# Optimization experiments

Measured on AMD Instinct MI355X. Metric: run time of the kernel, lower is better.

The kernel has to match this reference:

```python
import jax, jax.numpy as jnp
import numpy as np

N_QUBITS = 12
DEPTH = 4
OUT_DIM = 4096
BATCH = 2048
M_IN = 4096


def setup_inputs() -> dict:
    key = jax.random.key(0)
    k1, k2 = jax.random.split(key)
    x = jax.random.normal(k1, (BATCH, M_IN), dtype=jnp.float32)
    w = jax.random.uniform(k2, (DEPTH, N_QUBITS, 3), dtype=jnp.float32) * (2.0 * np.pi)
    return {"x": x, "w": w}


def _rot_matrix(phi, theta, omega):
    # PennyLane Rot(phi, theta, omega) = RZ(omega) @ RY(theta) @ RZ(phi)
    c = jnp.cos(theta / 2)
    s = jnp.sin(theta / 2)
    m = jnp.stack([
        jnp.stack([jnp.exp(-1j * (phi + omega) / 2) * c, -jnp.exp(1j * (phi - omega) / 2) * s]),
        jnp.stack([jnp.exp(-1j * (phi - omega) / 2) * s, jnp.exp(1j * (phi + omega) / 2) * c]),
    ])
    return m.astype(jnp.complex64)


def _apply_1q(s, U, q):
    # s: (B,) + (2,)*n ; wire q lives on axis q+1 (wire 0 = MSB, default.qubit order)
    s = jnp.moveaxis(s, q + 1, -1)
    s = jnp.einsum('...j,ij->...i', s, U)
    return jnp.moveaxis(s, -1, q + 1)


def _cnot(s, c, t):
    # control wire c < target wire t; flip target axis on the control=1 slice
    p0 = s[(slice(None),) * (c + 1) + (0,)]
    p1 = jnp.flip(s[(slice(None),) * (c + 1) + (1,)], axis=t)  # axis t after removing axis c+1
    return jnp.stack([p0, p1], axis=c + 1)


def _layer(s, wl):
    n = N_QUBITS
    for i in range(n):
        s = _apply_1q(s, _rot_matrix(wl[i, 0], wl[i, 1], wl[i, 2]), i)
    for i in range(n):
        for j in range(i + 1, n):
            s = _cnot(s, i, j)
    return s


def reference(x, w):
    B, m = x.shape
    n = N_QUBITS
    # amplitude embedding: per-sample L2 normalize with uniform fallback
    norm = jnp.linalg.norm(x, axis=1, keepdims=True)
    ok = norm > 1e-10
    amp = jnp.where(ok, x / jnp.where(ok, norm, 1.0), 1.0 / np.sqrt(m))
    s = amp.astype(jnp.complex64).reshape((B,) + (2,) * n)
    for layer in range(DEPTH):
        s = _layer(s, w[layer])
    sv = s.reshape(B, -1)
    probs = sv.real ** 2 + sv.imag ** 2
    pn = probs[:, :OUT_DIM]
    tot = jnp.sum(pn, axis=1, keepdims=True)
    okp = tot > 1e-10
    out = jnp.where(okp, pn / jnp.where(okp, tot, 1.0), 1.0 / OUT_DIM)
    return out.astype(x.dtype)
```

## Files before the change

### kernel.cpp

```cpp
#include <hip/hip_runtime.h>
#include <math.h>

#define NQ 12
#define DIM 4096
#define NLAYER 4
#define NT 256

typedef float v2 __attribute__((ext_vector_type(2)));

__device__ __forceinline__ v2 mkv2(float a, float b) { v2 r; r.x = a; r.y = b; return r; }
__device__ __forceinline__ v2 sp(float a) { v2 r; r.x = a; r.y = a; return r; }
__device__ __forceinline__ v2 pkfma(v2 a, float b, v2 c) {
  return __builtin_elementwise_fma(a, sp(b), c);
}

constexpr int sfun_c(int z) {
  z ^= z >> 1; z ^= z >> 2; z ^= z >> 4; z ^= z >> 8; return z & (DIM - 1);
}
constexpr int swz_c(int s) {
  int m = s ^ ((s >> 6) & 63);
  return m ^ ((m >> 3) & 7);
}
__device__ __forceinline__ int sfun(int z) {
  z ^= z >> 1; z ^= z >> 2; z ^= z >> 4; z ^= z >> 8; return z & (DIM - 1);
}
__device__ __forceinline__ int swz(int s) {
  int m = s ^ ((s >> 6) & 63);
  return m ^ ((m >> 3) & 7);
}

struct KT { int A[16], B[16], C[16], G[16]; };
constexpr KT mkKT() {
  KT k{};
  for (int j = 0; j < 16; ++j) {
    k.A[j] = swz_c(j << 8);
    k.B[j] = swz_c(j << 4);
    k.C[j] = swz_c(j);
    k.G[j] = swz_c(sfun_c(j << 8));
  }
  return k;
}
constexpr KT KTab = mkKT();

__device__ __forceinline__ v2 block_reduce_sum2(v2 v, v2* red) {
  const int tid = threadIdx.x;
#pragma unroll
  for (int off = 32; off > 0; off >>= 1) {
    v.x += __shfl_down(v.x, off, 64);
    v.y += __shfl_down(v.y, off, 64);
  }
  if ((tid & 63) == 0) red[tid >> 6] = v;
  __syncthreads();
  if (tid == 0) {
    v2 s = sp(0.f);
#pragma unroll
    for (int i = 0; i < NT / 64; ++i) s += red[i];
    red[0] = s;
  }
  __syncthreads();
  v2 r = red[0];
  __syncthreads();
  return r;
}

__device__ __forceinline__ void apply_pair(v2& r0, v2& i0, v2& r1, v2& i1,
    const float2 u00, const float2 u01, const float2 u10, const float2 u11) {
  v2 nr0 = pkfma(i1, -u01.y, pkfma(r1, u01.x, pkfma(i0, -u00.y, r0 * sp(u00.x))));
  v2 ni0 = pkfma(r1,  u01.y, pkfma(i1, u01.x, pkfma(r0,  u00.y, i0 * sp(u00.x))));
  v2 nr1 = pkfma(i1, -u11.y, pkfma(r1, u11.x, pkfma(i0, -u10.y, r0 * sp(u10.x))));
  v2 ni1 = pkfma(r1,  u11.y, pkfma(i1, u11.x, pkfma(r0,  u10.y, i0 * sp(u10.x))));
  r0 = nr0; i0 = ni0; r1 = nr1; i1 = ni1;
}

template <int QTOP>
__device__ __forceinline__ void gates4(v2 re[16], v2 im[16], const float2* GL) {
#pragma unroll
  for (int i = 0; i < 4; ++i) {
    const int q = QTOP - i;
    const float2 u00 = GL[q * 4 + 0], u01 = GL[q * 4 + 1];
    const float2 u10 = GL[q * 4 + 2], u11 = GL[q * 4 + 3];
#pragma unroll
    for (int pe = 0; pe < 8; ++pe) {
      const int e0 = ((pe >> i) << (i + 1)) | (pe & ((1 << i) - 1));
      const int e1 = e0 | (1 << i);
      apply_pair(re[e0], im[e0], re[e1], im[e1], u00, u01, u10, u11);
    }
  }
}

#define LOAD16(BASE, KARR)                        \
  _Pragma("unroll")                               \
  for (int j = 0; j < 16; ++j) {                  \
    const float4 v = st[(BASE) ^ KTab.KARR[j]];   \
    re[j] = mkv2(v.x, v.y);                       \
    im[j] = mkv2(v.z, v.w);                       \
  }
#define STORE16(BASE, KARR)                       \
  _Pragma("unroll")                               \
  for (int j = 0; j < 16; ++j)                    \
    st[(BASE) ^ KTab.KARR[j]] =                   \
        make_float4(re[j].x, re[j].y, im[j].x, im[j].y);

__global__ __launch_bounds__(NT, 2) void qsim_kernel(
    const float* __restrict__ x, const float* __restrict__ w,
    float* __restrict__ out) {
  extern __shared__ __align__(16) char smem[];
  float4* st   = (float4*)smem;
  float2* gmat = (float2*)(st + DIM);
  v2*     red  = (v2*)(gmat + NLAYER * NQ * 4);

  const int t = threadIdx.x;
  const int lane6 = t & 63, w2 = t >> 6;
  const long r0 = 2L * blockIdx.x;

  if (t < NLAYER * NQ) {
    const float* wp = w + t * 3;
    float phi = wp[0], th = wp[1], om = wp[2];
    float sn, cc, sa, ca, sb, cb;
    sincosf(0.5f * th, &sn, &cc);
    sincosf(0.5f * (phi + om), &sa, &ca);
    sincosf(0.5f * (phi - om), &sb, &cb);
    float2* g = &gmat[t * 4];
    g[0] = make_float2(ca * cc, -sa * cc);
    g[1] = make_float2(-cb * sn, -sb * sn);
    g[2] = make_float2(cb * sn, -sb * sn);
    g[3] = make_float2(ca * cc, sa * cc);
  }

  const float4* xa = (const float4*)(x + r0 * DIM) + t * 4;
  const float4* xb = (const float4*)(x + (r0 + 1) * DIM) + t * 4;
  float va[16], vb[16];
#pragma unroll
  for (int k = 0; k < 4; ++k) {
    const float4 A = xa[k], Bv = xb[k];
    va[k * 4 + 0] = A.x;  va[k * 4 + 1] = A.y;
    va[k * 4 + 2] = A.z;  va[k * 4 + 3] = A.w;
    vb[k * 4 + 0] = Bv.x; vb[k * 4 + 1] = Bv.y;
    vb[k * 4 + 2] = Bv.z; vb[k * 4 + 3] = Bv.w;
  }
  v2 ss = sp(0.f);
#pragma unroll
  for (int e = 0; e < 16; ++e) { ss.x += va[e] * va[e]; ss.y += vb[e] * vb[e]; }
  const v2 nsq = block_reduce_sum2(ss, red);
  const float n0 = sqrtf(nsq.x), n1 = sqrtf(nsq.y);
  const bool ok0 = n0 > 1e-10f, ok1 = n1 > 1e-10f;
  const float i0f = ok0 ? 1.0f / n0 : 0.f, i1f = ok1 ? 1.0f / n1 : 0.f;

  const int baseA = swz(t);
  const int baseB = swz((t & 15) | (w2 << 8) | (((t >> 4) & 3) << 10));
  const int baseC = swz((lane6 << 4) | (w2 << 10));
  const int gbase = swz(sfun(t));

#pragma unroll
  for (int e = 0; e < 16; ++e)
    st[baseC ^ KTab.C[e]] = make_float4(ok0 ? va[e] * i0f : 0.015625f,
                                        ok1 ? vb[e] * i1f : 0.015625f, 0.f, 0.f);
  __syncthreads();

  v2 re[16], im[16];
#pragma unroll
  for (int L = 0; L < NLAYER; ++L) {
    const float2* GL = &gmat[L * NQ * 4];

    if (L == 0) {
      LOAD16(baseA, A)
      gates4<3>(re, im, GL);
      STORE16(baseA, A)
    } else {
      LOAD16(gbase, G)
      gates4<3>(re, im, GL);
      __syncthreads();
      STORE16(baseA, A)
    }
    __syncthreads();

    LOAD16(baseB, B)
    gates4<7>(re, im, GL);
    STORE16(baseB, B)
    __syncthreads();

    LOAD16(baseC, C)
    gates4<11>(re, im, GL);
    STORE16(baseC, C)
    __syncthreads();
  }

  float q0[16], q1[16];
  v2 ps = sp(0.f);
#pragma unroll
  for (int k = 0; k < 16; ++k) {
    const float4 v = st[gbase ^ KTab.G[k]];
    q0[k] = v.x * v.x + v.z * v.z;
    q1[k] = v.y * v.y + v.w * v.w;
    ps.x += q0[k]; ps.y += q1[k];
  }
  const v2 tot = block_reduce_sum2(ps, red);
  const bool k0 = tot.x > 1e-10f, k1 = tot.y > 1e-10f;
  const float t0 = k0 ? 1.0f / tot.x : 0.f, t1 = k1 ? 1.0f / tot.y : 0.f;
  float* o0 = out + r0 * DIM;
  float* o1 = out + (r0 + 1) * DIM;
#pragma unroll
  for (int k = 0; k < 16; ++k) {
    o0[t + k * NT] = k0 ? q0[k] * t0 : (1.0f / DIM);
    o1[t + k * NT] = k1 ? q1[k] * t1 : (1.0f / DIM);
  }
}

extern "C" void kernel_launch(void* const* d_in, const int* in_sizes, int n_in,
                              void* d_out, int out_size, void* d_ws, size_t ws_size,
                              hipStream_t stream) {
  const float* x = (const float*)d_in[0];
  const float* w = (const float*)d_in[1];
  float* out = (float*)d_out;
  const int B = in_sizes[0] / DIM;
  const size_t smem = DIM * sizeof(float4) + NLAYER * NQ * 4 * sizeof(float2)
                    + (NT / 64) * sizeof(v2);
  qsim_kernel<<<B / 2, NT, smem, stream>>>(x, w, out);
}
```

Baseline: 87.71 us.

## Replace middle LDS transposition with permlane16/32 swaps, cutting shared-memory passes per layer

The three LDS load/store passes per layer become two. The qubits formerly covered by the middle pass are now applied through cross-lane exchanges using permlane16_swap and permlane32_swap, which move amplitude pairs between lanes in registers. The swizzle and the index mappings are redesigned to fit. A runtime probe detects the operand and result ordering of the swap intrinsic and dispatches to one of four template instantiations of the circuit. This removes shared-memory traffic and a barrier per layer, at the cost of extra permlane instructions, code size from four circuit copies, and a circuit loop that is no longer unrolled.

```diff
diff --git a/kernel.cpp b/kernel.cpp
--- a/kernel.cpp
+++ b/kernel.cpp
@@ -7,6 +7,7 @@
 #define NT 256
 
 typedef float v2 __attribute__((ext_vector_type(2)));
+typedef unsigned int u2 __attribute__((ext_vector_type(2)));
 
 __device__ __forceinline__ v2 mkv2(float a, float b) { v2 r; r.x = a; r.y = b; return r; }
 __device__ __forceinline__ v2 sp(float a) { v2 r; r.x = a; r.y = a; return r; }
@@ -14,29 +15,24 @@
   return __builtin_elementwise_fma(a, sp(b), c);
 }
 
-constexpr int sfun_c(int z) {
-  z ^= z >> 1; z ^= z >> 2; z ^= z >> 4; z ^= z >> 8; return z & (DIM - 1);
-}
-constexpr int swz_c(int s) {
-  int m = s ^ ((s >> 6) & 63);
-  return m ^ ((m >> 3) & 7);
-}
-__device__ __forceinline__ int sfun(int z) {
-  z ^= z >> 1; z ^= z >> 2; z ^= z >> 4; z ^= z >> 8; return z & (DIM - 1);
-}
-__device__ __forceinline__ int swz(int s) {
-  int m = s ^ ((s >> 6) & 63);
-  return m ^ ((m >> 3) & 7);
-}
-
-struct KT { int A[16], B[16], C[16], G[16]; };
+constexpr int sfun_c(int z) { z ^= z >> 1; z ^= z >> 2; z ^= z >> 4; z ^= z >> 8; return z & (DIM - 1); }
+constexpr int swz_mc(int z) {
+  const int h = (z >> 6) & 63;
+  return z ^ (h & 15) ^ ((h & 1) << 4) ^ ((h & 2) << 3) ^ ((h & 2) << 4);
+}
+__device__ __forceinline__ int sfun_d(int z) { z ^= z >> 1; z ^= z >> 2; z ^= z >> 4; z ^= z >> 8; return z & (DIM - 1); }
+__device__ __forceinline__ int swz_d(int z) {
+  const int h = (z >> 6) & 63;
+  return z ^ (h & 15) ^ ((h & 1) << 4) ^ ((h & 2) << 3) ^ ((h & 2) << 4);
+}
+
+struct KT { int P[16], Q[16], G[16]; };
 constexpr KT mkKT() {
   KT k{};
   for (int j = 0; j < 16; ++j) {
-    k.A[j] = swz_c(j << 8);
-    k.B[j] = swz_c(j << 4);
-    k.C[j] = swz_c(j);
-    k.G[j] = swz_c(sfun_c(j << 8));
+    k.P[j] = swz_mc(j << 8) << 4;
+    k.Q[j] = swz_mc(j) << 4;
+    k.G[j] = swz_mc(sfun_c(j << 8)) << 4;
   }
   return k;
 }
@@ -88,29 +84,96 @@
   }
 }
 
-#define LOAD16(BASE, KARR)                        \
-  _Pragma("unroll")                               \
-  for (int j = 0; j < 16; ++j) {                  \
-    const float4 v = st[(BASE) ^ KTab.KARR[j]];   \
-    re[j] = mkv2(v.x, v.y);                       \
-    im[j] = mkv2(v.z, v.w);                       \
-  }
-#define STORE16(BASE, KARR)                       \
-  _Pragma("unroll")                               \
-  for (int j = 0; j < 16; ++j)                    \
-    st[(BASE) ^ KTab.KARR[j]] =                   \
+template <int W, int AS, int RS>
+__device__ __forceinline__ void swap_one(float& a, float& b) {
+  const unsigned ua = __builtin_bit_cast(unsigned, a);
+  const unsigned ub = __builtin_bit_cast(unsigned, b);
+  u2 r;
+  if constexpr (W == 16)
+    r = __builtin_amdgcn_permlane16_swap(AS ? ub : ua, AS ? ua : ub, false, false);
+  else
+    r = __builtin_amdgcn_permlane32_swap(AS ? ub : ua, AS ? ua : ub, false, false);
+  a = __builtin_bit_cast(float, RS ? r[1] : r[0]);
+  b = __builtin_bit_cast(float, RS ? r[0] : r[1]);
+}
+
+template <int W, int AS, int RS>
+__device__ __forceinline__ void transpose_bit0(v2 re[16], v2 im[16]) {
+#pragma unroll
+  for (int k = 0; k < 8; ++k) {
+    float arx = re[2 * k].x, brx = re[2 * k + 1].x;
+    float ary = re[2 * k].y, bry = re[2 * k + 1].y;
+    float aix = im[2 * k].x, bix = im[2 * k + 1].x;
+    float aiy = im[2 * k].y, biy = im[2 * k + 1].y;
+    swap_one<W, AS, RS>(arx, brx);
+    swap_one<W, AS, RS>(ary, bry);
+    swap_one<W, AS, RS>(aix, bix);
+    swap_one<W, AS, RS>(aiy, biy);
+    re[2 * k] = mkv2(arx, ary); re[2 * k + 1] = mkv2(brx, bry);
+    im[2 * k] = mkv2(aix, aiy); im[2 * k + 1] = mkv2(bix, biy);
+  }
+}
+
+template <int W, int AS, int RS>
+__device__ __forceinline__ void lanegate(v2 re[16], v2 im[16], const float2* g) {
+  transpose_bit0<W, AS, RS>(re, im);
+  const float2 u00 = g[0], u01 = g[1], u10 = g[2], u11 = g[3];
+#pragma unroll
+  for (int k = 0; k < 8; ++k)
+    apply_pair(re[2 * k], im[2 * k], re[2 * k + 1], im[2 * k + 1], u00, u01, u10, u11);
+  transpose_bit0<W, AS, RS>(re, im);
+}
+
+#define LOAD16(BASE, KARR)                                             \
+  _Pragma("unroll")                                                    \
+  for (int j = 0; j < 16; ++j) {                                       \
+    const float4 v = *(const float4*)(st + ((BASE) ^ KTab.KARR[j]));   \
+    re[j] = mkv2(v.x, v.y);                                            \
+    im[j] = mkv2(v.z, v.w);                                            \
+  }
+#define STORE16(BASE, KARR)                                            \
+  _Pragma("unroll")                                                    \
+  for (int j = 0; j < 16; ++j)                                         \
+    *(float4*)(st + ((BASE) ^ KTab.KARR[j])) =                         \
         make_float4(re[j].x, re[j].y, im[j].x, im[j].y);
+
+template <int AS, int RS>
+__device__ __forceinline__ void circuit(char* st, const float2* gmat,
+                                        int basePb, int baseQb, int gbaseb) {
+  v2 re[16], im[16];
+  for (int L = 0; L < NLAYER; ++L) {
+    const float2* GL = &gmat[L * NQ * 4];
+    if (L == 0) {
+      LOAD16(basePb, P)
+    } else {
+      LOAD16(gbaseb, G)
+    }
+    gates4<3>(re, im, GL);
+    lanegate<16, AS, RS>(re, im, &GL[5 * 4]);
+    lanegate<32, AS, RS>(re, im, &GL[4 * 4]);
+    if (L > 0) __syncthreads();
+    STORE16(basePb, P)
+    __syncthreads();
+
+    LOAD16(baseQb, Q)
+    gates4<11>(re, im, GL);
+    lanegate<16, AS, RS>(re, im, &GL[7 * 4]);
+    lanegate<32, AS, RS>(re, im, &GL[6 * 4]);
+    STORE16(baseQb, Q)
+    __syncthreads();
+  }
+}
 
 __global__ __launch_bounds__(NT, 2) void qsim_kernel(
     const float* __restrict__ x, const float* __restrict__ w,
     float* __restrict__ out) {
   extern __shared__ __align__(16) char smem[];
-  float4* st   = (float4*)smem;
-  float2* gmat = (float2*)(st + DIM);
+  char*   st   = smem;
+  float2* gmat = (float2*)(smem + DIM * 16);
   v2*     red  = (v2*)(gmat + NLAYER * NQ * 4);
 
   const int t = threadIdx.x;
-  const int lane6 = t & 63, w2 = t >> 6;
+  const int lane = t & 63, w2 = t >> 6;
   const long r0 = 2L * blockIdx.x;
 
   if (t < NLAYER * NQ) {
@@ -146,50 +209,45 @@
   const bool ok0 = n0 > 1e-10f, ok1 = n1 > 1e-10f;
   const float i0f = ok0 ? 1.0f / n0 : 0.f, i1f = ok1 ? 1.0f / n1 : 0.f;
 
-  const int baseA = swz(t);
-  const int baseB = swz((t & 15) | (w2 << 8) | (((t >> 4) & 3) << 10));
-  const int baseC = swz((lane6 << 4) | (w2 << 10));
-  const int gbase = swz(sfun(t));
+  const int zP = (lane & 15) | (w2 << 4) | ((lane >> 4) << 6);
+  const int basePb = swz_d(zP) << 4;
+  const int baseQb = swz_d(((lane >> 4) << 4) | ((lane & 15) << 6) | (w2 << 10)) << 4;
+  const int gbaseb = swz_d(sfun_d(zP)) << 4;
+  const int baseEb = swz_d(t << 4) << 4;
+  const int obaseb = swz_d(sfun_d(t)) << 4;
 
 #pragma unroll
   for (int e = 0; e < 16; ++e)
-    st[baseC ^ KTab.C[e]] = make_float4(ok0 ? va[e] * i0f : 0.015625f,
-                                        ok1 ? vb[e] * i1f : 0.015625f, 0.f, 0.f);
-  __syncthreads();
-
-  v2 re[16], im[16];
-#pragma unroll
-  for (int L = 0; L < NLAYER; ++L) {
-    const float2* GL = &gmat[L * NQ * 4];
-
-    if (L == 0) {
-      LOAD16(baseA, A)
-      gates4<3>(re, im, GL);
-      STORE16(baseA, A)
-    } else {
-      LOAD16(gbase, G)
-      gates4<3>(re, im, GL);
-      __syncthreads();
-      STORE16(baseA, A)
-    }
-    __syncthreads();
-
-    LOAD16(baseB, B)
-    gates4<7>(re, im, GL);
-    STORE16(baseB, B)
-    __syncthreads();
-
-    LOAD16(baseC, C)
-    gates4<11>(re, im, GL);
-    STORE16(baseC, C)
-    __syncthreads();
+    *(float4*)(st + (baseEb ^ KTab.Q[e])) =
+        make_float4(ok0 ? va[e] * i0f : 0.015625f,
+                    ok1 ? vb[e] * i1f : 0.015625f, 0.f, 0.f);
+  __syncthreads();
+
+  bool asw, rsw;
+  {
+    const float px = (lane & 16) ? 2.f : 0.f;
+    const float py = px + 1.f;
+    const u2 pr = __builtin_amdgcn_permlane16_swap(
+        __builtin_bit_cast(unsigned, px), __builtin_bit_cast(unsigned, py),
+        false, false);
+    const float v0 = __shfl(__builtin_bit_cast(float, pr[0]), 16, 64);
+    const float v1 = __shfl(__builtin_bit_cast(float, pr[1]), 16, 64);
+    asw = (v0 == 0.f || v0 == 3.f);
+    rsw = asw ? (v0 == 3.f) : (v0 == 2.f);
+  }
+  if (asw) {
+    if (rsw) circuit<1, 1>(st, gmat, basePb, baseQb, gbaseb);
+    else     circuit<1, 0>(st, gmat, basePb, baseQb, gbaseb);
+  } else {
+    if (rsw) circuit<0, 1>(st, gmat, basePb, baseQb, gbaseb);
+    else     circuit<0, 0>(st, gmat, basePb, baseQb, gbaseb);
   }
 
   float q0[16], q1[16];
   v2 ps = sp(0.f);
 #pragma unroll
   for (int k = 0; k < 16; ++k) {
-    const float4 v = st[gbase ^ KTab.G[k]];
+    const float4 v = *(const float4*)(st + (obaseb ^ KTab.G[k]));
     q0[k] = v.x * v.x + v.z * v.z;
     q1[k] = v.y * v.y + v.w * v.w;
     ps.x += q0[k]; ps.y += q1[k];
@@ -213,7 +271,7 @@
   const float* w = (const float*)d_in[1];
   float* out = (float*)d_out;
   const int B = in_sizes[0] / DIM;
-  const size_t smem = DIM * sizeof(float4) + NLAYER * NQ * 4 * sizeof(float2)
+  const size_t smem = DIM * 16 + NLAYER * NQ * 4 * sizeof(float2)
                     + (NT / 64) * sizeof(v2);
   qsim_kernel<<<B / 2, NT, smem, stream>>>(x, w, out);
 }
```

Result: slower. 93.87 us (+7.0%).
